# Optimization experiments

Hardware: AMD Instinct MI355X
Metric: run time of the kernel (lower is better)

Reference implementation:

```python
import jax, jax.numpy as jnp
import numpy as np

N_NODES = 50000
N_EDGES = 1600000
NFEAT, NHID, NCLASS = 512, 256, 40


def _spmm(edge_src, edge_dst, edge_vals, h):
    # out[i] = sum_{e: dst[e]==i} vals[e] * h[src[e]]
    msgs = edge_vals[:, None] * h[edge_src]  # [E, D]
    return jax.ops.segment_sum(msgs, edge_dst, num_segments=h.shape[0])


def _gc(edge_src, edge_dst, edge_vals, x, W, b):
    # GraphConvolution: adj @ (x @ W) + b
    return _spmm(edge_src, edge_dst, edge_vals, x @ W) + b


def setup_inputs() -> dict:
    key = jax.random.key(0)
    ks = jax.random.split(key, 16)
    s = 0.05
    return {
        "x": jax.random.normal(ks[0], (N_NODES, NFEAT), jnp.float32),
        "edge_src": jax.random.randint(ks[1], (N_EDGES,), 0, N_NODES, jnp.int32),
        "edge_dst": jax.random.randint(ks[2], (N_EDGES,), 0, N_NODES, jnp.int32),
        "edge_vals": jax.random.uniform(ks[3], (N_EDGES,), jnp.float32),
        "W0": jax.random.normal(ks[4], (NFEAT, NHID), jnp.float32) * s,
        "b0": jax.random.normal(ks[5], (NHID,), jnp.float32) * s,
        "W1": jax.random.normal(ks[6], (NFEAT, NHID), jnp.float32) * s,
        "b1": jax.random.normal(ks[7], (NHID,), jnp.float32) * s,
        "W2": jax.random.normal(ks[8], (NHID, NHID), jnp.float32) * s,
        "b2": jax.random.normal(ks[9], (NHID,), jnp.float32) * s,
        "W3": jax.random.normal(ks[10], (NHID, NHID), jnp.float32) * s,
        "b3": jax.random.normal(ks[11], (NHID,), jnp.float32) * s,
        "W5": jax.random.normal(ks[12], (4 * NHID, NCLASS), jnp.float32) * s,
        "b5": jax.random.normal(ks[13], (NCLASS,), jnp.float32) * s,
    }


def reference(x, edge_src, edge_dst, edge_vals, W0, b0, W1, b1, W2, b2, W3, b3, W5, b5):
    z = x @ W0 + b0
    x1 = jax.nn.relu(_gc(edge_src, edge_dst, edge_vals, x, W1, b1)) + z
    # NOTE: the original module applies gc2 (same weights) twice; gc4 is unused.
    x2 = jax.nn.relu(_gc(edge_src, edge_dst, edge_vals, x1, W2, b2)) + x1
    x3 = jax.nn.relu(_gc(edge_src, edge_dst, edge_vals, x2, W2, b2)) + x2
    x4 = jax.nn.relu(_gc(edge_src, edge_dst, edge_vals, x3, W3, b3)) + x3
    xc = jnp.concatenate((x4, x3, x2, x1), axis=1)  # [N, 4*nhid]
    # dropout is identity in eval mode
    x5 = _gc(edge_src, edge_dst, edge_vals, xc, W5, b5)
    return jax.nn.log_softmax(x5, axis=1)
```

## Files before the change

### kernel.cpp

```cpp
#include <hip/hip_runtime.h>
#include <hip/hip_fp16.h>
#include <math.h>
#include <stdint.h>

#define N_NODES 50000
#define N_EDGES 1600000
#define NFEAT 512
#define NHID 256
#define NCLASS 40
#define MPAD 50048
#define NPART 8
#define PEDGE 200000
#define PCAP 212992
#define EPB2 1024
#define BPP 128
#define NBLK 196
#define SLICE_STRIDE ((size_t)MPAD * 32)
#define CEV_CAP 6144

typedef _Float16 half8 __attribute__((ext_vector_type(8)));
typedef float floatx4 __attribute__((ext_vector_type(4)));

__device__ __forceinline__ void gload_lds16(const void* g, void* l) {
    __builtin_amdgcn_global_load_lds((const __attribute__((address_space(1))) void*)g,
                                     (__attribute__((address_space(3))) void*)l, 16, 0, 0);
}

__device__ __forceinline__ float cev_val(unsigned ev) {
    return (float)__builtin_bit_cast(_Float16, (unsigned short)(ev >> 16));
}


__global__ void zero_i32(int* __restrict__ p, int n) {
    int i = blockIdx.x * blockDim.x + threadIdx.x;
    if (i < n) p[i] = 0;
}

__global__ void hist_kernel(const int* __restrict__ dst, int* __restrict__ cnt) {
    int i = blockIdx.x * blockDim.x + threadIdx.x;
    int stride = gridDim.x * blockDim.x;
    for (; i < N_EDGES; i += stride) atomicAdd(&cnt[dst[i]], 1);
}

__global__ __launch_bounds__(1024) void exscan4_kernel(const int* __restrict__ cnt,
                                                       int* __restrict__ rowptr,
                                                       int* __restrict__ cursor, int n) {
    __shared__ int wsum[16];
    __shared__ int carry_s;
    const int tid = threadIdx.x;
    const int lane = tid & 63;
    const int wid = tid >> 6;
    if (tid == 0) carry_s = 0;
    __syncthreads();
    for (int base = 0; base < n; base += 4096) {
        int i0 = base + tid * 4;
        int4 v = make_int4(0, 0, 0, 0);
        if (i0 + 3 < n) {
            v = *(const int4*)(cnt + i0);
        } else {
            if (i0 + 0 < n) v.x = cnt[i0 + 0];
            if (i0 + 1 < n) v.y = cnt[i0 + 1];
            if (i0 + 2 < n) v.z = cnt[i0 + 2];
        }
        int s = v.x + v.y + v.z + v.w;
        int sc = s;
        #pragma unroll
        for (int off = 1; off < 64; off <<= 1) {
            int t = __shfl_up(sc, off);
            if (lane >= off) sc += t;
        }
        if (lane == 63) wsum[wid] = sc;
        __syncthreads();
        if (wid == 0) {
            int ws = (lane < 16) ? wsum[lane] : 0;
            #pragma unroll
            for (int off = 1; off < 16; off <<= 1) {
                int t = __shfl_up(ws, off);
                if (lane >= off) ws += t;
            }
            if (lane < 16) wsum[lane] = ws;
        }
        __syncthreads();
        int ex = carry_s + (wid ? wsum[wid - 1] : 0) + sc - s;
        int p0 = ex, p1 = ex + v.x, p2 = p1 + v.y, p3 = p2 + v.z;
        if (i0 + 0 < n) { rowptr[i0 + 0] = p0; if (cursor) cursor[i0 + 0] = p0; }
        if (i0 + 1 < n) { rowptr[i0 + 1] = p1; if (cursor) cursor[i0 + 1] = p1; }
        if (i0 + 2 < n) { rowptr[i0 + 2] = p2; if (cursor) cursor[i0 + 2] = p2; }
        if (i0 + 3 < n) { rowptr[i0 + 3] = p3; if (cursor) cursor[i0 + 3] = p3; }
        __syncthreads();
        if (tid == 0) carry_s += wsum[15];
        __syncthreads();
    }
    if (tid == 0) rowptr[n] = carry_s;
}

__global__ __launch_bounds__(1024) void exscan4g_kernel(const int* __restrict__ cnt,
                                                        const int* __restrict__ order,
                                                        int* __restrict__ rowptr,
                                                        int* __restrict__ cursor, int n) {
    __shared__ int wsum[16];
    __shared__ int carry_s;
    const int tid = threadIdx.x;
    const int lane = tid & 63;
    const int wid = tid >> 6;
    if (tid == 0) carry_s = 0;
    __syncthreads();
    for (int base = 0; base < n; base += 4096) {
        int i0 = base + tid * 4;
        int4 v = make_int4(0, 0, 0, 0);
        if (i0 + 0 < n) v.x = cnt[order[i0 + 0]];
        if (i0 + 1 < n) v.y = cnt[order[i0 + 1]];
        if (i0 + 2 < n) v.z = cnt[order[i0 + 2]];
        if (i0 + 3 < n) v.w = cnt[order[i0 + 3]];
        int s = v.x + v.y + v.z + v.w;
        int sc = s;
        #pragma unroll
        for (int off = 1; off < 64; off <<= 1) {
            int t = __shfl_up(sc, off);
            if (lane >= off) sc += t;
        }
        if (lane == 63) wsum[wid] = sc;
        __syncthreads();
        if (wid == 0) {
            int ws = (lane < 16) ? wsum[lane] : 0;
            #pragma unroll
            for (int off = 1; off < 16; off <<= 1) {
                int t = __shfl_up(ws, off);
                if (lane >= off) ws += t;
            }
            if (lane < 16) wsum[lane] = ws;
        }
        __syncthreads();
        int ex = carry_s + (wid ? wsum[wid - 1] : 0) + sc - s;
        int p0 = ex, p1 = ex + v.x, p2 = p1 + v.y, p3 = p2 + v.z;
        if (i0 + 0 < n) { rowptr[i0 + 0] = p0; cursor[i0 + 0] = p0; }
        if (i0 + 1 < n) { rowptr[i0 + 1] = p1; cursor[i0 + 1] = p1; }
        if (i0 + 2 < n) { rowptr[i0 + 2] = p2; cursor[i0 + 2] = p2; }
        if (i0 + 3 < n) { rowptr[i0 + 3] = p3; cursor[i0 + 3] = p3; }
        __syncthreads();
        if (tid == 0) carry_s += wsum[15];
        __syncthreads();
    }
    if (tid == 0) rowptr[n] = carry_s;
}


__global__ __launch_bounds__(256) void sort_hist_kernel(const int* __restrict__ cnt,
                                                        int* __restrict__ gh) {
    __shared__ int lbin[256];
    int t = threadIdx.x;
    lbin[t] = 0;
    __syncthreads();
    int i = blockIdx.x * 256 + t;
    if (i < N_NODES) atomicAdd(&lbin[255 - min(cnt[i], 255)], 1);
    __syncthreads();
    gh[t * NBLK + blockIdx.x] = lbin[t];
}

__global__ __launch_bounds__(256) void sort_scatter_kernel(const int* __restrict__ cnt,
                                                           const int* __restrict__ ghx,
                                                           int* __restrict__ order,
                                                           int* __restrict__ rank) {
    __shared__ int lbase[256], lcnt2[256];
    int t = threadIdx.x;
    lbase[t] = ghx[t * NBLK + blockIdx.x];
    lcnt2[t] = 0;
    __syncthreads();
    int i = blockIdx.x * 256 + t;
    if (i < N_NODES) {
        int bin = 255 - min(cnt[i], 255);
        int my = atomicAdd(&lcnt2[bin], 1);
        int pos = lbase[bin] + my;
        order[pos] = i;
        rank[i] = pos;
    }
}


__global__ __launch_bounds__(256) void bin2_kernel(const int* __restrict__ esrc,
                                                   const int* __restrict__ edst,
                                                   const float* __restrict__ evals,
                                                   const int* __restrict__ rank,
                                                   const int* __restrict__ rowptr,
                                                   int* __restrict__ pcount,
                                                   uint2* __restrict__ plist) {
    __shared__ int lcnt[NPART], lbase[NPART], lcur[NPART];
    const int base = blockIdx.x * EPB2;
    const int n = min(EPB2, N_EDGES - base);
    const int tid = threadIdx.x;
    const int lane = tid & 63;
    if (tid < NPART) { lcnt[tid] = 0; lcur[tid] = 0; }
    __syncthreads();
    for (int i = tid; i < n; i += 256) {
        int rd = rank[edst[base + i]];
        int p = rowptr[rd] / PEDGE;
        atomicAdd(&lcnt[p], 1);
    }
    __syncthreads();
    if (tid < NPART) lbase[tid] = atomicAdd(&pcount[tid], lcnt[tid]);
    __syncthreads();
    const int nceil = (n + 255) & ~255;
    for (int i = tid; i < nceil; i += 256) {
        bool on = i < n;
        int d = 0, s = 0; float v = 0.f;
        if (on) { d = edst[base + i]; s = esrc[base + i]; v = evals[base + i]; }
        int rd = on ? rank[d] : 0;
        int rs = on ? rank[s] : 0;
        int p = on ? (rowptr[rd] / PEDGE) : NPART;
        int mybase = 0, myoff = 0;
        #pragma unroll
        for (int q = 0; q < NPART; ++q) {
            unsigned long long mq = __ballot(p == q);
            int cq = __popcll(mq);
            int wbq = 0;
            if (lane == q && cq > 0) wbq = atomicAdd(&lcur[q], cq);
            wbq = __shfl(wbq, q);
            if (p == q) {
                mybase = wbq;
                myoff = __popcll(mq & ((1ull << lane) - 1ull));
            }
        }
        if (on) {
            plist[(size_t)p * PCAP + lbase[p] + mybase + myoff] =
                make_uint2(((unsigned)rd << 16) | (unsigned)rs, __float_as_uint(v));
        }
    }
}

__global__ __launch_bounds__(256) void pscatter2_kernel(const int* __restrict__ pcount,
                                                        const uint2* __restrict__ plist,
                                                        int* __restrict__ cursor,
                                                        unsigned* __restrict__ cev) {
    int part = blockIdx.x & (NPART - 1);
    int bip = blockIdx.x >> 3;
    int n = pcount[part];
    const uint2* lp = plist + (size_t)part * PCAP;
    for (int i = bip * 256 + threadIdx.x; i < n; i += BPP * 256) {
        uint2 r = lp[i];
        int rd = r.x >> 16;
        int rs = r.x & 0xFFFF;
        int pos = atomicAdd(&cursor[rd], 1);
        unsigned short hb = __builtin_bit_cast(unsigned short, (_Float16)__uint_as_float(r.y));
        cev[pos] = ((unsigned)hb << 16) | (unsigned)rs;
    }
}


__global__ void conv_w_kernel(const float* __restrict__ W, _Float16* __restrict__ BT,
                              int K, int N, int Npad) {
    int id = blockIdx.x * blockDim.x + threadIdx.x;
    if (id >= Npad * K) return;
    int n = id / K;
    int k = id - n * K;
    BT[id] = (n < N) ? (_Float16)W[(size_t)k * N + n] : (_Float16)0.f;
}

__global__ __launch_bounds__(256) void conv_xs(const float* __restrict__ x,
                                               const int* __restrict__ rank,
                                               _Float16* __restrict__ xh) {
    int id = blockIdx.x * 256 + threadIdx.x;
    int node = id >> 6;
    int kc = (id & 63) * 8;
    if (node >= MPAD) return;
    half8 h;
    if (node < N_NODES) {
        const float4* p = (const float4*)(x + (size_t)node * NFEAT + kc);
        float4 a = p[0], b = p[1];
        h[0] = (_Float16)a.x; h[1] = (_Float16)a.y; h[2] = (_Float16)a.z; h[3] = (_Float16)a.w;
        h[4] = (_Float16)b.x; h[5] = (_Float16)b.y; h[6] = (_Float16)b.z; h[7] = (_Float16)b.w;
        int pos = rank[node];
        __builtin_nontemporal_store(h, (half8*)(xh + (size_t)pos * NFEAT + kc));
    } else {
        #pragma unroll
        for (int j = 0; j < 8; ++j) h[j] = (_Float16)0.f;
        *(half8*)(xh + (size_t)node * NFEAT + kc) = h;
    }
}


__global__ __launch_bounds__(256, 2)
void gemm_x16(const _Float16* __restrict__ A, const _Float16* __restrict__ BT,
              const float* __restrict__ bias1,
              _Float16* __restrict__ out1, _Float16* __restrict__ out2) {
    __shared__ _Float16 As[128 * 64];
    __shared__ _Float16 Bs[128 * 64];

    const int tid = threadIdx.x;
    const int w = tid >> 6;
    const int lane = tid & 63;
    const int row0 = blockIdx.y * 128;
    const int col0 = blockIdx.x * 128;

    const int wr = w >> 1;
    const int wc = w & 1;
    const int mi = lane & 15;
    const int ksel = lane >> 4;

    const int srow = lane >> 3;
    const int scol = ((lane & 7) ^ srow) << 3;

    floatx4 acc[4][4];
    #pragma unroll
    for (int i = 0; i < 4; ++i)
        #pragma unroll
        for (int j = 0; j < 4; ++j)
            acc[i][j] = (floatx4)0.f;

    for (int k0 = 0; k0 < NFEAT; k0 += 64) {
        #pragma unroll
        for (int j = 0; j < 4; ++j) {
            int rowblk = (j * 4 + w) * 8;
            const _Float16* src = A + (size_t)(row0 + rowblk + srow) * NFEAT + k0 + scol;
            gload_lds16(src, (char*)As + rowblk * 128);
        }
        #pragma unroll
        for (int j = 0; j < 4; ++j) {
            int nblk = (j * 4 + w) * 8;
            const _Float16* src = BT + (size_t)(col0 + nblk + srow) * NFEAT + k0 + scol;
            gload_lds16(src, (char*)Bs + nblk * 128);
        }
        asm volatile("s_waitcnt vmcnt(0)" ::: "memory");
        __syncthreads();

        half8 a[2][4];
        half8 b[2][4];
        #pragma unroll
        for (int kk = 0; kk < 2; ++kk) {
            int kb = kk * 64 + (ksel << 4);
            #pragma unroll
            for (int fm = 0; fm < 4; ++fm) {
                int r = wr * 64 + fm * 16 + mi;
                int byte = kb ^ ((r & 7) << 4);
                a[kk][fm] = *(const half8*)((const char*)As + r * 128 + byte);
            }
            #pragma unroll
            for (int fn = 0; fn < 4; ++fn) {
                int n = wc * 64 + fn * 16 + mi;
                int byte = kb ^ ((n & 7) << 4);
                b[kk][fn] = *(const half8*)((const char*)Bs + n * 128 + byte);
            }
        }
        #pragma unroll
        for (int kk = 0; kk < 2; ++kk)
            #pragma unroll
            for (int fm = 0; fm < 4; ++fm)
                #pragma unroll
                for (int fn = 0; fn < 4; ++fn)
                    acc[fm][fn] = __builtin_amdgcn_mfma_f32_16x16x32_f16(
                        a[kk][fm], b[kk][fn], acc[fm][fn], 0, 0, 0);
        __syncthreads();
    }

    #pragma unroll
    for (int fm = 0; fm < 4; ++fm) {
        #pragma unroll
        for (int fn = 0; fn < 4; ++fn) {
            #pragma unroll
            for (int r = 0; r < 4; ++r) {
                int gr = row0 + wr * 64 + fm * 16 + (lane >> 4) * 4 + r;
                int gc = col0 + wc * 64 + fn * 16 + (lane & 15);
                if (gr < N_NODES) {
                    float v = acc[fm][fn][r];
                    if (gc < 256) {
                        out1[(size_t)(gc >> 5) * SLICE_STRIDE + (size_t)gr * 32 + (gc & 31)] =
                            (_Float16)(v + bias1[gc]);
                    } else {
                        int gc2 = gc - 256;
                        out2[(size_t)(gc2 >> 5) * SLICE_STRIDE + (size_t)gr * 32 + (gc2 & 31)] =
                            (_Float16)v;
                    }
                }
            }
        }
    }
}


template<int BN, bool OUTS>
__global__ __launch_bounds__(256, 2)
void gemm_f16(const _Float16* __restrict__ A0, const _Float16* __restrict__ A1,
              const _Float16* __restrict__ A2, const _Float16* __restrict__ A3,
              int kPerPart, int K,
              const _Float16* __restrict__ BT,
              _Float16* __restrict__ out1, int M, int N) {
    constexpr int WN = BN / 2;
    constexpr int FN = WN / 16;
    __shared__ _Float16 As[128 * 64];
    __shared__ _Float16 Bs[BN * 64];

    const int tid = threadIdx.x;
    const int w = tid >> 6;
    const int lane = tid & 63;
    const int row0 = blockIdx.y * 128;
    const int col0 = blockIdx.x * BN;

    const int wr = w >> 1;
    const int wc = w & 1;
    const int mi = lane & 15;
    const int ksel = lane >> 4;

    const int srow = lane >> 3;
    const int gsw = (lane & 7) ^ srow;

    floatx4 acc[4][FN];
    #pragma unroll
    for (int i = 0; i < 4; ++i)
        #pragma unroll
        for (int j = 0; j < FN; ++j)
            acc[i][j] = (floatx4)0.f;

    for (int k0 = 0; k0 < K; k0 += 64) {
        int part = k0 / kPerPart;
        int kloc = k0 - part * kPerPart;
        const _Float16* Ap = (part == 0) ? A0 : (part == 1) ? A1 : (part == 2) ? A2 : A3;
        int sA0 = kloc >> 5;

        #pragma unroll
        for (int j = 0; j < 4; ++j) {
            int chunk = j * 4 + w;
            int r = chunk * 8 + srow;
            const _Float16* src = Ap + (size_t)(sA0 + (gsw >> 2)) * SLICE_STRIDE
                                + (size_t)(row0 + r) * 32 + (gsw & 3) * 8;
            gload_lds16(src, (char*)As + chunk * 1024);
        }
        #pragma unroll
        for (int j = 0; j < BN / 32; ++j) {
            int nblk = (j * 4 + w) * 8;
            const _Float16* src = BT + (size_t)(col0 + nblk + srow) * K + k0 + ((lane & 7) ^ srow) * 8;
            gload_lds16(src, (char*)Bs + nblk * 128);
        }
        asm volatile("s_waitcnt vmcnt(0)" ::: "memory");
        __syncthreads();

        half8 a[2][4];
        half8 b[2][FN];
        #pragma unroll
        for (int kk = 0; kk < 2; ++kk) {
            int kb = kk * 64 + (ksel << 4);
            #pragma unroll
            for (int fm = 0; fm < 4; ++fm) {
                int r = wr * 64 + fm * 16 + mi;
                int byte = kb ^ ((r & 7) << 4);
                a[kk][fm] = *(const half8*)((const char*)As + r * 128 + byte);
            }
            #pragma unroll
            for (int fn = 0; fn < FN; ++fn) {
                int n = wc * WN + fn * 16 + mi;
                int byte = kb ^ ((n & 7) << 4);
                b[kk][fn] = *(const half8*)((const char*)Bs + n * 128 + byte);
            }
        }
        #pragma unroll
        for (int kk = 0; kk < 2; ++kk)
            #pragma unroll
            for (int fm = 0; fm < 4; ++fm)
                #pragma unroll
                for (int fn = 0; fn < FN; ++fn)
                    acc[fm][fn] = __builtin_amdgcn_mfma_f32_16x16x32_f16(
                        a[kk][fm], b[kk][fn], acc[fm][fn], 0, 0, 0);
        __syncthreads();
    }

    #pragma unroll
    for (int fm = 0; fm < 4; ++fm) {
        #pragma unroll
        for (int fn = 0; fn < FN; ++fn) {
            #pragma unroll
            for (int r = 0; r < 4; ++r) {
                int gr = row0 + wr * 64 + fm * 16 + (lane >> 4) * 4 + r;
                int gc = col0 + wc * WN + fn * 16 + (lane & 15);
                if (gr < M && gc < N) {
                    float v = acc[fm][fn][r];
                    if (OUTS) {
                        out1[(size_t)(gc >> 5) * SLICE_STRIDE + (size_t)gr * 32 + (gc & 31)] =
                            (_Float16)v;
                    } else {
                        out1[(size_t)gr * N + gc] = (_Float16)v;
                    }
                }
            }
        }
    }
}


#define SPMM_EDGE_LOOP(EVSRC)                                                     \
    for (int e = 0; __any(e < deg); e += 8) {                                     \
        unsigned ev[8];                                                           \
        _Pragma("unroll")                                                         \
        for (int u = 0; u < 8; ++u) {                                             \
            int ee = e + u;                                                       \
            ev[u] = EVSRC(begs + (ee < deg ? ee : 0));                            \
        }                                                                         \
        uint4 hw[8];                                                              \
        _Pragma("unroll")                                                         \
        for (int u = 0; u < 8; ++u)                                               \
            hw[u] = *(const uint4*)(Y + (size_t)(ev[u] & 0xFFFF) * 32);           \
        _Pragma("unroll")                                                         \
        for (int u = 0; u < 8; ++u) {                                             \
            unsigned short vb = (e + u < deg) ? (unsigned short)(ev[u] >> 16)     \
                                              : (unsigned short)0;                \
            __half vh = __builtin_bit_cast(__half, vb);                           \
            __half2 vv = __half2half2(vh);                                        \
            ac0 = __hfma2(vv, __builtin_bit_cast(__half2, hw[u].x), ac0);         \
            ac1 = __hfma2(vv, __builtin_bit_cast(__half2, hw[u].y), ac1);         \
            ac2 = __hfma2(vv, __builtin_bit_cast(__half2, hw[u].z), ac2);         \
            ac3 = __hfma2(vv, __builtin_bit_cast(__half2, hw[u].w), ac3);         \
        }                                                                         \
    }

__global__ __launch_bounds__(256) void spmm_epi_sl(const int* __restrict__ rowptr,
                                                   const unsigned* __restrict__ cev,
                                                   const _Float16* __restrict__ Ysl,
                                                   const float* __restrict__ bias,
                                                   const _Float16* __restrict__ ressl,
                                                   _Float16* __restrict__ outsl) {
    __shared__ unsigned sev[CEV_CAP];
    __shared__ int srp[65];
    const int tid = threadIdx.x;
    const int w = tid >> 6;
    const int lane = tid & 63;
    const int slice = blockIdx.x & 7;
    const int rb = (blockIdx.x >> 3) * 64;

    if (tid < 65) srp[tid] = rowptr[min(rb + tid, N_NODES)];
    __syncthreads();
    const int ebase = srp[0];
    const int ecnt = srp[64] - ebase;
    const int nstage = min(ecnt, CEV_CAP);
    for (int i = tid; i < nstage; i += 256) sev[i] = cev[ebase + i];
    __syncthreads();

    const int lrow = w * 16 + (lane >> 2);
    const int rowIdx = rb + lrow;
    const int fl = (lane & 3) * 8;
    const _Float16* Y = Ysl + (size_t)slice * SLICE_STRIDE + fl;

    bool active = rowIdx < N_NODES;
    int deg = srp[lrow + 1] - srp[lrow];
    int begs = (deg > 0) ? (srp[lrow] - ebase) : 0;

    __half2 ac0 = __float2half2_rn(0.f), ac1 = ac0, ac2 = ac0, ac3 = ac0;
    if (ecnt <= CEV_CAP) {
        #define EV_LDS(i) sev[(i)]
        SPMM_EDGE_LOOP(EV_LDS)
        #undef EV_LDS
    } else {
        #define EV_GLB(i) cev[ebase + (i)]
        SPMM_EDGE_LOOP(EV_GLB)
        #undef EV_GLB
    }
    if (active) {
        int col = slice * 32 + fl;
        float4 bb0 = *(const float4*)(bias + col);
        float4 bb1 = *(const float4*)(bias + col + 4);
        size_t ro = (size_t)slice * SLICE_STRIDE + (size_t)rowIdx * 32 + fl;
        half8 rr = __builtin_nontemporal_load((const half8*)(ressl + ro));
        float2 f0 = __half22float2(ac0), f1 = __half22float2(ac1);
        float2 f2 = __half22float2(ac2), f3 = __half22float2(ac3);
        half8 o;
        o[0] = (_Float16)(fmaxf(f0.x + bb0.x, 0.f) + (float)rr[0]);
        o[1] = (_Float16)(fmaxf(f0.y + bb0.y, 0.f) + (float)rr[1]);
        o[2] = (_Float16)(fmaxf(f1.x + bb0.z, 0.f) + (float)rr[2]);
        o[3] = (_Float16)(fmaxf(f1.y + bb0.w, 0.f) + (float)rr[3]);
        o[4] = (_Float16)(fmaxf(f2.x + bb1.x, 0.f) + (float)rr[4]);
        o[5] = (_Float16)(fmaxf(f2.y + bb1.y, 0.f) + (float)rr[5]);
        o[6] = (_Float16)(fmaxf(f3.x + bb1.z, 0.f) + (float)rr[6]);
        o[7] = (_Float16)(fmaxf(f3.y + bb1.w, 0.f) + (float)rr[7]);
        __builtin_nontemporal_store(o, (half8*)(outsl + ro));
    }
}


__global__ __launch_bounds__(256) void spmm40_lsm(const int* __restrict__ rowptr,
                                                  const int* __restrict__ order,
                                                  const unsigned* __restrict__ cev,
                                                  const _Float16* __restrict__ Y5,
                                                  const float* __restrict__ bias,
                                                  float* __restrict__ out) {
    int rowIdx = (blockIdx.x * blockDim.x + threadIdx.x) >> 6;
    if (rowIdx >= N_NODES) return;
    int lane = threadIdx.x & 63;
    bool act = lane < NCLASS;
    const _Float16* Yl = Y5 + lane;
    int row = order[rowIdx];
    int beg = rowptr[rowIdx];
    int end = rowptr[rowIdx + 1];
    float acc = 0.f;
    int e = beg;
    for (; e + 8 <= end; e += 8) {
        unsigned ev[8];
        #pragma unroll
        for (int j = 0; j < 8; ++j) ev[j] = cev[e + j];
        float h[8];
        #pragma unroll
        for (int j = 0; j < 8; ++j)
            h[j] = act ? (float)Yl[(size_t)(ev[j] & 0xFFFF) * NCLASS] : 0.f;
        #pragma unroll
        for (int j = 0; j < 8; ++j) acc = fmaf(cev_val(ev[j]), h[j], acc);
    }
    for (; e < end; ++e) {
        unsigned ev = cev[e];
        float h = act ? (float)Yl[(size_t)(ev & 0xFFFF) * NCLASS] : 0.f;
        acc = fmaf(cev_val(ev), h, acc);
    }
    float x = act ? (acc + bias[lane]) : -INFINITY;
    float m = x;
    #pragma unroll
    for (int off = 32; off > 0; off >>= 1) m = fmaxf(m, __shfl_xor(m, off));
    float ex = act ? __expf(x - m) : 0.f;
    float ssum = ex;
    #pragma unroll
    for (int off = 32; off > 0; off >>= 1) ssum += __shfl_xor(ssum, off);
    float ls = logf(ssum);
    if (act) out[(size_t)row * NCLASS + lane] = x - m - ls;
}


extern "C" void kernel_launch(void* const* d_in, const int* in_sizes, int n_in,
                              void* d_out, int out_size, void* d_ws, size_t ws_size,
                              hipStream_t stream) {
    const float* x     = (const float*)d_in[0];
    const int*   esrc  = (const int*)d_in[1];
    const int*   edst  = (const int*)d_in[2];
    const float* evals = (const float*)d_in[3];
    const float* W0 = (const float*)d_in[4];
    const float* b0 = (const float*)d_in[5];
    const float* W1 = (const float*)d_in[6];
    const float* b1 = (const float*)d_in[7];
    const float* W2 = (const float*)d_in[8];
    const float* b2 = (const float*)d_in[9];
    const float* W3 = (const float*)d_in[10];
    const float* b3 = (const float*)d_in[11];
    const float* W5 = (const float*)d_in[12];
    const float* b5 = (const float*)d_in[13];
    float* out = (float*)d_out;

    char* ws = (char*)d_ws;
    size_t off = 0;
    auto alloc = [&](size_t bytes) {
        char* p = ws + off;
        off = (off + bytes + 255) & ~(size_t)255;
        return p;
    };
    const size_t SLB = 2ull * 8 * SLICE_STRIDE;
    _Float16* xh   = (_Float16*)alloc(2ull * MPAD * NFEAT);
    _Float16* zh   = (_Float16*)alloc(SLB);
    _Float16* Yh   = (_Float16*)alloc(SLB);
    _Float16* x1h  = (_Float16*)alloc(SLB);
    _Float16* x2h  = (_Float16*)alloc(SLB);
    _Float16* x3h  = (_Float16*)alloc(SLB);
    _Float16* x4h  = (_Float16*)alloc(SLB);
    _Float16* Y5h  = (_Float16*)alloc(2ull * N_NODES * NCLASS);
    _Float16* BT01 = (_Float16*)alloc(2ull * 512 * NFEAT);
    _Float16* BT2  = (_Float16*)alloc(2ull * NHID * NHID);
    _Float16* BT3  = (_Float16*)alloc(2ull * NHID * NHID);
    _Float16* BT5  = (_Float16*)alloc(2ull * 64 * 1024);
    int* cnt    = (int*)alloc(sizeof(int) * (N_NODES + NPART));
    int* pcount = cnt + N_NODES;
    int* gh     = (int*)alloc(sizeof(int) * (NBLK * 256));
    int* ghx    = (int*)alloc(sizeof(int) * (NBLK * 256 + 1));
    int* order  = (int*)alloc(sizeof(int) * N_NODES);
    int* rank   = (int*)alloc(sizeof(int) * N_NODES);
    int* rowptr = (int*)alloc(sizeof(int) * (N_NODES + 1));
    int* cursor = (int*)alloc(sizeof(int) * N_NODES);
    uint2* plist = (uint2*)alloc(8ull * NPART * PCAP);
    unsigned* cev = (unsigned*)alloc(4ull * N_EDGES + 256);
    (void)ws_size;

    zero_i32<<<(N_NODES + NPART + 255) / 256, 256, 0, stream>>>(cnt, N_NODES + NPART);
    hist_kernel<<<2048, 256, 0, stream>>>(edst, cnt);
    sort_hist_kernel<<<NBLK, 256, 0, stream>>>(cnt, gh);
    exscan4_kernel<<<1, 1024, 0, stream>>>(gh, ghx, nullptr, NBLK * 256);
    sort_scatter_kernel<<<NBLK, 256, 0, stream>>>(cnt, ghx, order, rank);
    exscan4g_kernel<<<1, 1024, 0, stream>>>(cnt, order, rowptr, cursor, N_NODES);
    bin2_kernel<<<(N_EDGES + EPB2 - 1) / EPB2, 256, 0, stream>>>(esrc, edst, evals, rank, rowptr, pcount, plist);
    pscatter2_kernel<<<NPART * BPP, 256, 0, stream>>>(pcount, plist, cursor, cev);

    conv_xs<<<MPAD / 4, 256, 0, stream>>>(x, rank, xh);
    conv_w_kernel<<<(256 * NFEAT + 255) / 256, 256, 0, stream>>>(W0, BT01, NFEAT, NHID, NHID);
    conv_w_kernel<<<(256 * NFEAT + 255) / 256, 256, 0, stream>>>(W1, BT01 + 256 * NFEAT, NFEAT, NHID, NHID);
    conv_w_kernel<<<(NHID * NHID + 255) / 256, 256, 0, stream>>>(W2, BT2, NHID, NHID, NHID);
    conv_w_kernel<<<(NHID * NHID + 255) / 256, 256, 0, stream>>>(W3, BT3, NHID, NHID, NHID);
    conv_w_kernel<<<(64 * 1024 + 255) / 256, 256, 0, stream>>>(W5, BT5, 1024, NCLASS, 64);

    const int mtiles = MPAD / 128;
    const int spmmGrid = ((N_NODES + 63) / 64) * 8;
    dim3 blk(256);

    gemm_x16<<<dim3(4, mtiles), blk, 0, stream>>>(xh, BT01, b0, zh, Yh);
    spmm_epi_sl<<<spmmGrid, blk, 0, stream>>>(rowptr, cev, Yh, b1, zh, x1h);

    gemm_f16<128, true><<<dim3(2, mtiles), blk, 0, stream>>>(x1h, x1h, x1h, x1h, NHID, NHID, BT2, Yh, N_NODES, NHID);
    spmm_epi_sl<<<spmmGrid, blk, 0, stream>>>(rowptr, cev, Yh, b2, x1h, x2h);

    gemm_f16<128, true><<<dim3(2, mtiles), blk, 0, stream>>>(x2h, x2h, x2h, x2h, NHID, NHID, BT2, Yh, N_NODES, NHID);
    spmm_epi_sl<<<spmmGrid, blk, 0, stream>>>(rowptr, cev, Yh, b2, x2h, x3h);

    gemm_f16<128, true><<<dim3(2, mtiles), blk, 0, stream>>>(x3h, x3h, x3h, x3h, NHID, NHID, BT3, Yh, N_NODES, NHID);
    spmm_epi_sl<<<spmmGrid, blk, 0, stream>>>(rowptr, cev, Yh, b3, x3h, x4h);

    gemm_f16<64, false><<<dim3(1, mtiles), blk, 0, stream>>>(x4h, x3h, x2h, x1h, NHID, 4 * NHID, BT5, Y5h, N_NODES, NCLASS);

    spmm40_lsm<<<(N_NODES * 64 + 255) / 256, blk, 0, stream>>>(rowptr, order, cev, Y5h, b5, out);
}
```

Measured before the change: 816.1 us.

## Pack five lanes per row in final SpMM and stage edge lists in LDS

```diff
diff --git a/kernel.cpp b/kernel.cpp
--- a/kernel.cpp
+++ b/kernel.cpp
@@ -17,6 +17,7 @@
 #define NBLK 196
 #define SLICE_STRIDE ((size_t)MPAD * 32)
 #define CEV_CAP 6144
+#define R40 48
 
 typedef _Float16 half8 __attribute__((ext_vector_type(8)));
 typedef float floatx4 __attribute__((ext_vector_type(4)));
@@ -191,38 +192,42 @@
     const int lane = tid & 63;
     if (tid < NPART) { lcnt[tid] = 0; lcur[tid] = 0; }
     __syncthreads();
-    for (int i = tid; i < n; i += 256) {
-        int rd = rank[edst[base + i]];
-        int p = rowptr[rd] / PEDGE;
-        atomicAdd(&lcnt[p], 1);
+    int rd[4], rs[4], p[4];
+    float v[4];
+    #pragma unroll
+    for (int j = 0; j < 4; ++j) {
+        int i = tid + j * 256;
+        bool on = i < n;
+        int d = on ? edst[base + i] : 0;
+        int s = on ? esrc[base + i] : 0;
+        v[j] = on ? evals[base + i] : 0.f;
+        rd[j] = on ? rank[d] : 0;
+        rs[j] = on ? rank[s] : 0;
+        p[j] = on ? (rowptr[rd[j]] / PEDGE) : NPART;
+        if (on) atomicAdd(&lcnt[p[j]], 1);
     }
     __syncthreads();
     if (tid < NPART) lbase[tid] = atomicAdd(&pcount[tid], lcnt[tid]);
     __syncthreads();
-    const int nceil = (n + 255) & ~255;
-    for (int i = tid; i < nceil; i += 256) {
-        bool on = i < n;
-        int d = 0, s = 0; float v = 0.f;
-        if (on) { d = edst[base + i]; s = esrc[base + i]; v = evals[base + i]; }
-        int rd = on ? rank[d] : 0;
-        int rs = on ? rank[s] : 0;
-        int p = on ? (rowptr[rd] / PEDGE) : NPART;
+    #pragma unroll
+    for (int j = 0; j < 4; ++j) {
+        int pp = p[j];
         int mybase = 0, myoff = 0;
         #pragma unroll
         for (int q = 0; q < NPART; ++q) {
-            unsigned long long mq = __ballot(p == q);
+            unsigned long long mq = __ballot(pp == q);
             int cq = __popcll(mq);
             int wbq = 0;
             if (lane == q && cq > 0) wbq = atomicAdd(&lcur[q], cq);
             wbq = __shfl(wbq, q);
-            if (p == q) {
+            if (pp == q) {
                 mybase = wbq;
                 myoff = __popcll(mq & ((1ull << lane) - 1ull));
             }
         }
-        if (on) {
-            plist[(size_t)p * PCAP + lbase[p] + mybase + myoff] =
-                make_uint2(((unsigned)rd << 16) | (unsigned)rs, __float_as_uint(v));
+        if (pp < NPART) {
+            plist[(size_t)pp * PCAP + lbase[pp] + mybase + myoff] =
+                make_uint2(((unsigned)rd[j] << 16) | (unsigned)rs[j], __float_as_uint(v[j]));
         }
     }
 }
@@ -572,48 +577,94 @@
 }
 
 
+#define SPMM40_LOOP(EVSRC)                                                        \
+    for (int e = 0; __any(e < deg); e += 4) {                                     \
+        unsigned ev[4];                                                           \
+        _Pragma("unroll")                                                         \
+        for (int u = 0; u < 4; ++u) {                                             \
+            int ee = e + u;                                                       \
+            ev[u] = EVSRC(begs + (ee < deg ? ee : 0));                            \
+        }                                                                         \
+        uint4 hw[4];                                                              \
+        _Pragma("unroll")                                                         \
+        for (int u = 0; u < 4; ++u)                                               \
+            hw[u] = *(const uint4*)(Y5 + (size_t)(ev[u] & 0xFFFF) * NCLASS + sub * 8); \
+        _Pragma("unroll")                                                         \
+        for (int u = 0; u < 4; ++u) {                                             \
+            float v = (e + u < deg) ? cev_val(ev[u]) : 0.f;                       \
+            const _Float16* hp = (const _Float16*)&hw[u];                         \
+            _Pragma("unroll")                                                     \
+            for (int j = 0; j < 8; ++j) acc[j] = fmaf(v, (float)hp[j], acc[j]);   \
+        }                                                                         \
+    }
+
 __global__ __launch_bounds__(256) void spmm40_lsm(const int* __restrict__ rowptr,
                                                   const int* __restrict__ order,
                                                   const unsigned* __restrict__ cev,
                                                   const _Float16* __restrict__ Y5,
                                                   const float* __restrict__ bias,
                                                   float* __restrict__ out) {
-    int rowIdx = (blockIdx.x * blockDim.x + threadIdx.x) >> 6;
-    if (rowIdx >= N_NODES) return;
-    int lane = threadIdx.x & 63;
-    bool act = lane < NCLASS;
-    const _Float16* Yl = Y5 + lane;
-    int row = order[rowIdx];
-    int beg = rowptr[rowIdx];
-    int end = rowptr[rowIdx + 1];
-    float acc = 0.f;
-    int e = beg;
-    for (; e + 8 <= end; e += 8) {
-        unsigned ev[8];
-        #pragma unroll
-        for (int j = 0; j < 8; ++j) ev[j] = cev[e + j];
-        float h[8];
-        #pragma unroll
-        for (int j = 0; j < 8; ++j)
-            h[j] = act ? (float)Yl[(size_t)(ev[j] & 0xFFFF) * NCLASS] : 0.f;
-        #pragma unroll
-        for (int j = 0; j < 8; ++j) acc = fmaf(cev_val(ev[j]), h[j], acc);
-    }
-    for (; e < end; ++e) {
-        unsigned ev = cev[e];
-        float h = act ? (float)Yl[(size_t)(ev & 0xFFFF) * NCLASS] : 0.f;
-        acc = fmaf(cev_val(ev), h, acc);
-    }
-    float x = act ? (acc + bias[lane]) : -INFINITY;
-    float m = x;
-    #pragma unroll
-    for (int off = 32; off > 0; off >>= 1) m = fmaxf(m, __shfl_xor(m, off));
-    float ex = act ? __expf(x - m) : 0.f;
-    float ssum = ex;
-    #pragma unroll
-    for (int off = 32; off > 0; off >>= 1) ssum += __shfl_xor(ssum, off);
-    float ls = logf(ssum);
-    if (act) out[(size_t)row * NCLASS + lane] = x - m - ls;
+    __shared__ unsigned sev[CEV_CAP];
+    __shared__ int srp[R40 + 1];
+    const int tid = threadIdx.x;
+    const int w = tid >> 6;
+    const int lane = tid & 63;
+    const int rb = blockIdx.x * R40;
+
+    if (tid < R40 + 1) srp[tid] = rowptr[min(rb + tid, N_NODES)];
+    __syncthreads();
+    const int ebase = srp[0];
+    const int ecnt = srp[R40] - ebase;
+    const int nstage = min(ecnt, CEV_CAP);
+    for (int i = tid; i < nstage; i += 256) sev[i] = cev[ebase + i];
+    __syncthreads();
+
+    const int g = lane / 5;
+    const int sub = lane - g * 5;
+    const int lrow = w * 12 + g;
+    const int rowIdx = rb + lrow;
+    bool active = (g < 12) && (rowIdx < N_NODES);
+    int deg = active ? (srp[lrow + 1] - srp[lrow]) : 0;
+    int begs = active ? (srp[lrow] - ebase) : 0;
+
+    float acc[8] = {};
+    if (ecnt <= CEV_CAP) {
+        #define EV_LDS(i) sev[(i)]
+        SPMM40_LOOP(EV_LDS)
+        #undef EV_LDS
+    } else {
+        #define EV_GLB(i) cev[ebase + (i)]
+        SPMM40_LOOP(EV_GLB)
+        #undef EV_GLB
+    }
+
+    if (active) {
+        float xv[8];
+        #pragma unroll
+        for (int j = 0; j < 8; ++j) xv[j] = acc[j] + bias[sub * 8 + j];
+        float m = xv[0];
+        #pragma unroll
+        for (int j = 1; j < 8; ++j) m = fmaxf(m, xv[j]);
+        float gm = m;
+        #pragma unroll
+        for (int k = 0; k < 5; ++k) gm = fmaxf(gm, __shfl(m, g * 5 + k));
+        float s = 0.f;
+        #pragma unroll
+        for (int j = 0; j < 8; ++j) s += __expf(xv[j] - gm);
+        float gs = 0.f;
+        #pragma unroll
+        for (int k = 0; k < 5; ++k) gs += __shfl(s, g * 5 + k);
+        float ls = logf(gs);
+        int row = order[rowIdx];
+        float* op = out + (size_t)row * NCLASS + sub * 8;
+        float4 o0, o1;
+        o0.x = xv[0] - gm - ls; o0.y = xv[1] - gm - ls;
+        o0.z = xv[2] - gm - ls; o0.w = xv[3] - gm - ls;
+        o1.x = xv[4] - gm - ls; o1.y = xv[5] - gm - ls;
+        o1.z = xv[6] - gm - ls; o1.w = xv[7] - gm - ls;
+        *(float4*)(op + 0) = o0;
+        *(float4*)(op + 4) = o1;
+    }
 }
 
 
@@ -702,5 +753,5 @@
 
     gemm_f16<64, false><<<dim3(1, mtiles), blk, 0, stream>>>(x4h, x3h, x2h, x1h, NHID, 4 * NHID, BT5, Y5h, N_NODES, NCLASS);
 
-    spmm40_lsm<<<(N_NODES * 64 + 255) / 256, blk, 0, stream>>>(rowptr, order, cev, Y5h, b5, out);
-}
+    spmm40_lsm<<<(N_NODES + R40 - 1) / R40, blk, 0, stream>>>(rowptr, order, cev, Y5h, b5, out);
+}
```

Result: faster. 735.9 us (-9.8%).
